# Optimization experiments

Measured on AMD Instinct MI355X. Metric: run time of the kernel, lower is better.

## Reference

```python
import jax, jax.numpy as jnp
from jax import lax
import numpy as np

B, N, C = 64, 8732, 81  # batch, anchors (SSD300), classes (COCO+bg)
POS_RATE = 0.003        # keep 3*num_pos < N (argsort column index must be in range)


def setup_inputs() -> dict:
    key = jax.random.key(0)
    k1, k2, k3, k4, k5, k6 = jax.random.split(key, 6)
    pred_conf = jax.random.normal(k1, (B, N, C), dtype=jnp.float32)
    pred_loc = jax.random.normal(k2, (B, N, 4), dtype=jnp.float32)
    # one-hot gt_conf; class 0 = background; sparse positives
    is_pos = jax.random.uniform(k3, (B, N)) < POS_RATE
    labels = jnp.where(is_pos, jax.random.randint(k4, (B, N), 1, C), 0)
    gt_conf = jax.nn.one_hot(labels, C, dtype=jnp.float32)
    gt_loc = jax.random.normal(k5, (B, N, 4), dtype=jnp.float32)
    return {"pred_conf": pred_conf, "pred_loc": pred_loc,
            "gt_conf": gt_conf, "gt_loc": gt_loc}


def reference(pred_conf, pred_loc, gt_conf, gt_loc):
    negative_ratio = 3.0
    # softmax cross entropy per anchor: [B, N]
    log_sm = jax.nn.log_softmax(pred_conf, axis=-1)
    conf_loss = -jnp.sum(log_sm * gt_conf, axis=-1)

    # positive mask (gt background prob == 0 => positive); detached in original
    pos_mask = (lax.stop_gradient(gt_conf)[:, :, 0] == 0).astype(jnp.float32)
    num_pos = jnp.sum(pos_mask)
    positive_conf_loss = pos_mask * conf_loss

    # hard-negative mining (faithful to original, including the quirk that the
    # "threshold" is the argsort INDEX value at column num_negative_conf)
    neg_mask = 1.0 - pos_mask
    cl_neg = lax.stop_gradient(conf_loss) * neg_mask  # detached in original
    order = jnp.argsort(cl_neg, axis=-1)              # [B, N] ascending
    num_neg = (negative_ratio * num_pos).astype(jnp.int32)  # scalar, traced
    idx = jnp.broadcast_to(num_neg, (cl_neg.shape[0], 1))
    thr = jnp.take_along_axis(order, idx, axis=1).astype(jnp.float32)  # [B,1]
    neg_mask = neg_mask * (cl_neg > thr).astype(jnp.float32)
    negative_conf_loss = neg_mask * conf_loss

    conf_total = jnp.sum(positive_conf_loss + negative_conf_loss, axis=-1)  # [B]

    # smooth-L1-ish loc loss (faithful, incl. loc_loss_mask == linear mask bug)
    d = pred_loc - gt_loc
    lin = (jnp.abs(lax.stop_gradient(d)) > 1.0).astype(jnp.float32)
    loc = ((jnp.abs(d) - 0.5) * lin + 0.5 * d * d * (1.0 - lin)) * lin
    loc_total = jnp.sum(loc, axis=(-1, -2))  # [B]

    return conf_total, loc_total
```

## Files before the change

kernel.cpp:

```cpp
#include <hip/hip_runtime.h>
#include <hip/hip_bf16.h>
#include <math.h>

#define NCLS 81
#define NANCH 8732
#define NB 64
#define TILE_A 64
#define TILE_FLOATS (TILE_A * NCLS)
#define NBUCKET 64
#define BUCKET_STRIDE 16

__global__ __launch_bounds__(256) void conf_kernel(
    const float* __restrict__ pred_conf,
    const float* __restrict__ gt_conf,
    float* __restrict__ val_out,
    int* __restrict__ pos_buckets)
{
    __shared__ float sp[TILE_FLOATS];
    __shared__ float sg[TILE_FLOATS];
    __shared__ int pcnt[4];
    const int tid = threadIdx.x;
    const long long tile = blockIdx.x;
    const long long base = tile * (long long)TILE_FLOATS;

    const float4* p4 = (const float4*)(pred_conf + base);
    const float4* g4 = (const float4*)(gt_conf + base);
    float4* sp4 = (float4*)sp;
    float4* sg4 = (float4*)sg;
#pragma unroll
    for (int i = 0; i < 6; ++i) {
        int idx = tid + i * 256;
        if (idx < TILE_FLOATS / 4) {
            sp4[idx] = p4[idx];
            sg4[idx] = g4[idx];
        }
    }
    __syncthreads();

    const int a = tid >> 2;
    const int q = tid & 3;
    const float* xrow = sp + a * NCLS;
    const float* grow = sg + a * NCLS;

    float x[21];
    float m = -INFINITY;
#pragma unroll
    for (int j = 0; j < 21; ++j) {
        int c = q + 4 * j;
        x[j] = (c < NCLS) ? xrow[c] : -INFINITY;
        m = fmaxf(m, x[j]);
    }
    m = fmaxf(m, __shfl_xor(m, 1));
    m = fmaxf(m, __shfl_xor(m, 2));

    float s = 0.f;
#pragma unroll
    for (int j = 0; j < 21; ++j) {
        int c = q + 4 * j;
        if (c < NCLS) s += expf(x[j] - m);
    }
    s += __shfl_xor(s, 1);
    s += __shfl_xor(s, 2);
    const float lse = m + logf(s);

    float dot = 0.f;
#pragma unroll
    for (int j = 0; j < 21; ++j) {
        int c = q + 4 * j;
        if (c < NCLS) dot += (x[j] - lse) * grow[c];
    }
    dot += __shfl_xor(dot, 1);
    dot += __shfl_xor(dot, 2);
    const float conf_loss = -dot;

    bool pos = false;
    if (q == 0) {
        pos = (grow[0] == 0.0f);
        val_out[tile * TILE_A + a] = pos ? -conf_loss : conf_loss;
    }
    unsigned long long mb = __ballot(pos);
    if ((tid & 63) == 0) pcnt[tid >> 6] = (int)__popcll(mb);
    __syncthreads();
    if (tid == 0) {
        int tot = pcnt[0] + pcnt[1] + pcnt[2] + pcnt[3];
        if (tot)
            atomicAdd(&pos_buckets[(blockIdx.x & (NBUCKET - 1)) * BUCKET_STRIDE], tot);
    }
}

__global__ __launch_bounds__(256) void loc_kernel(
    const float* __restrict__ pred_loc,
    const float* __restrict__ gt_loc,
    float* __restrict__ out)
{
    __shared__ float red[4];
    const int b = blockIdx.y;
    const int idx = blockIdx.x * 256 + threadIdx.x;
    float local = 0.f;
    if (idx < NANCH) {
        const float4* p = (const float4*)(pred_loc + (long long)b * (NANCH * 4));
        const float4* g = (const float4*)(gt_loc + (long long)b * (NANCH * 4));
        float4 pv = p[idx];
        float4 gv = g[idx];
        float d0 = pv.x - gv.x, d1 = pv.y - gv.y, d2 = pv.z - gv.z, d3 = pv.w - gv.w;
        float a0 = fabsf(d0), a1 = fabsf(d1), a2 = fabsf(d2), a3 = fabsf(d3);
        local  = (a0 > 1.f) ? (a0 - 0.5f) : 0.f;
        local += (a1 > 1.f) ? (a1 - 0.5f) : 0.f;
        local += (a2 > 1.f) ? (a2 - 0.5f) : 0.f;
        local += (a3 > 1.f) ? (a3 - 0.5f) : 0.f;
    }
    for (int off = 32; off; off >>= 1) local += __shfl_xor(local, off);
    if ((threadIdx.x & 63) == 0) red[threadIdx.x >> 6] = local;
    __syncthreads();
    if (threadIdx.x == 0)
        atomicAdd(&out[64 + b], red[0] + red[1] + red[2] + red[3]);
}

__global__ __launch_bounds__(256) void select_kernel(
    const float* __restrict__ val,
    const int* __restrict__ pos_buckets,
    float* __restrict__ out)
{
    __shared__ float cl[NANCH];
    __shared__ int hist[256];
    __shared__ int wsum[4];
    __shared__ int sh_numpos;
    __shared__ unsigned int sh_prefix;
    __shared__ int sh_k, sh_thr;
    __shared__ float red[4];

    const int b = blockIdx.x;
    const int tid = threadIdx.x;
    const int lane = tid & 63, w = tid >> 6;
    const float* row = val + (long long)b * NANCH;

    if (tid < 64) {
        int v = pos_buckets[tid * BUCKET_STRIDE];
        for (int off = 32; off; off >>= 1) v += __shfl_xor(v, off);
        if (tid == 0) sh_numpos = v;
    }

    float pos_local = 0.f;
    for (int i = tid; i < NANCH; i += 256) {
        float v = row[i];
        cl[i] = fmaxf(v, 0.0f);
        if (v < 0.f) pos_local -= v;
    }
    __syncthreads();

    int k = 3 * sh_numpos;
    if (k > NANCH - 1) k = NANCH - 1;
    if (k < 0) k = 0;

    unsigned int prefix = 0u;
    for (int r = 0; r < 4; ++r) {
        const int shift = 24 - 8 * r;
        const unsigned int maskHigh = (r == 0) ? 0u : (0xFFFFFFFFu << (shift + 8));
        hist[tid] = 0;
        __syncthreads();
        for (int i = tid; i < NANCH; i += 256) {
            unsigned int u = __float_as_uint(cl[i]);
            if ((u & maskHigh) == prefix)
                atomicAdd(&hist[(u >> shift) & 0xFF], 1);
        }
        __syncthreads();
        int h = hist[tid];
        int v = h;
#pragma unroll
        for (int off = 1; off < 64; off <<= 1) {
            int u2 = __shfl_up(v, off);
            if (lane >= off) v += u2;
        }
        if (lane == 63) wsum[w] = v;
        __syncthreads();
        int add = 0;
        for (int i = 0; i < w; ++i) add += wsum[i];
        int incl = v + add, excl = incl - h;
        if (excl <= k && k < incl) {
            sh_prefix = prefix | ((unsigned int)tid << shift);
            sh_k = k - excl;
        }
        __syncthreads();
        prefix = sh_prefix;
        k = sh_k;
        __syncthreads();
    }
    const unsigned int T = prefix;

    const int CHUNK = (NANCH + 255) / 256;
    const int lo = tid * CHUNK;
    const int hi = (lo + CHUNK < NANCH) ? (lo + CHUNK) : NANCH;
    int cnt = 0;
    for (int i = lo; i < hi; ++i)
        if (__float_as_uint(cl[i]) == T) ++cnt;
    {
        int v = cnt;
#pragma unroll
        for (int off = 1; off < 64; off <<= 1) {
            int u2 = __shfl_up(v, off);
            if (lane >= off) v += u2;
        }
        if (lane == 63) wsum[w] = v;
        __syncthreads();
        int add = 0;
        for (int i = 0; i < w; ++i) add += wsum[i];
        int incl = v + add, excl = incl - cnt;
        if (excl <= k && k < incl) {
            int need = k - excl, idx = NANCH - 1;
            for (int i = lo; i < hi; ++i) {
                if (__float_as_uint(cl[i]) == T) {
                    if (need == 0) { idx = i; break; }
                    --need;
                }
            }
            sh_thr = idx;
        }
        __syncthreads();
    }

    const float thr = (float)sh_thr;
    float local = pos_local;
    for (int i = tid; i < NANCH; i += 256) {
        float c = cl[i];
        if (c > thr) local += c;
    }
    for (int off = 32; off; off >>= 1) local += __shfl_xor(local, off);
    if ((tid & 63) == 0) red[tid >> 6] = local;
    __syncthreads();
    if (tid == 0) out[b] = red[0] + red[1] + red[2] + red[3];
}

extern "C" void kernel_launch(void* const* d_in, const int* in_sizes, int n_in,
                              void* d_out, int out_size, void* d_ws, size_t ws_size,
                              hipStream_t stream) {
    const float* pred_conf = (const float*)d_in[0];
    const float* pred_loc  = (const float*)d_in[1];
    const float* gt_conf   = (const float*)d_in[2];
    const float* gt_loc    = (const float*)d_in[3];
    float* out = (float*)d_out;

    int*   pos_buckets = (int*)d_ws;
    float* vals        = (float*)((char*)d_ws + 8192);

    hipMemsetAsync(d_ws, 0, 8192, stream);
    hipMemsetAsync(d_out, 0, 128 * sizeof(float), stream);

    conf_kernel<<<NB * NANCH / TILE_A, 256, 0, stream>>>(pred_conf, gt_conf, vals, pos_buckets);
    loc_kernel<<<dim3((NANCH + 255) / 256, NB), 256, 0, stream>>>(pred_loc, gt_loc, out);
    select_kernel<<<NB, 256, 0, stream>>>(vals, pos_buckets, out);
}
```

Measured before the change: 427.6 us.

## Drop LDS staging in conf kernel, atomically accumulate positive loss, widen select blocks

The conf kernel no longer stages tiles of pred_conf and gt_conf in shared memory. Each thread now reads its strided classes straight from global memory, which removes the LDS footprint and a barrier but gives up coalesced float4 loads. Positive-anchor losses are reduced per wavefront and added atomically into a per-row buffer, so the select kernel can load clean values without separating signs. The select kernel runs with 1024 threads per block to parallelise the radix-select passes across the 64 rows, at the cost of more barrier overhead.

New measurement: 404.3 us. 5.5% less time.

```diff
diff --git a/kernel.cpp b/kernel.cpp
--- a/kernel.cpp
+++ b/kernel.cpp
@@ -5,42 +5,20 @@
 #define NCLS 81
 #define NANCH 8732
 #define NB 64
-#define TILE_A 64
-#define TILE_FLOATS (TILE_A * NCLS)
-#define NBUCKET 64
 #define BUCKET_STRIDE 16
 
 __global__ __launch_bounds__(256) void conf_kernel(
     const float* __restrict__ pred_conf,
     const float* __restrict__ gt_conf,
-    float* __restrict__ val_out,
-    int* __restrict__ pos_buckets)
+    float* __restrict__ cl_out,
+    int* __restrict__ pos_buckets,
+    float* __restrict__ row_pos)
 {
-    __shared__ float sp[TILE_FLOATS];
-    __shared__ float sg[TILE_FLOATS];
-    __shared__ int pcnt[4];
     const int tid = threadIdx.x;
-    const long long tile = blockIdx.x;
-    const long long base = tile * (long long)TILE_FLOATS;
-
-    const float4* p4 = (const float4*)(pred_conf + base);
-    const float4* g4 = (const float4*)(gt_conf + base);
-    float4* sp4 = (float4*)sp;
-    float4* sg4 = (float4*)sg;
-#pragma unroll
-    for (int i = 0; i < 6; ++i) {
-        int idx = tid + i * 256;
-        if (idx < TILE_FLOATS / 4) {
-            sp4[idx] = p4[idx];
-            sg4[idx] = g4[idx];
-        }
-    }
-    __syncthreads();
-
-    const int a = tid >> 2;
+    const int anchor = blockIdx.x * 64 + (tid >> 2);
     const int q = tid & 3;
-    const float* xrow = sp + a * NCLS;
-    const float* grow = sg + a * NCLS;
+    const float* xrow = pred_conf + (size_t)anchor * NCLS;
+    const float* grow = gt_conf + (size_t)anchor * NCLS;
 
     float x[21];
     float m = -INFINITY;
@@ -63,28 +41,37 @@
     s += __shfl_xor(s, 2);
     const float lse = m + logf(s);
 
-    float dot = 0.f;
+    float dot = 0.f, g0 = 1.f;
 #pragma unroll
     for (int j = 0; j < 21; ++j) {
         int c = q + 4 * j;
-        if (c < NCLS) dot += (x[j] - lse) * grow[c];
+        if (c < NCLS) {
+            float g = grow[c];
+            if (c == 0) g0 = g;
+            dot = fmaf(g, x[j] - lse, dot);
+        }
     }
     dot += __shfl_xor(dot, 1);
     dot += __shfl_xor(dot, 2);
     const float conf_loss = -dot;
 
-    bool pos = false;
-    if (q == 0) {
-        pos = (grow[0] == 0.0f);
-        val_out[tile * TILE_A + a] = pos ? -conf_loss : conf_loss;
-    }
-    unsigned long long mb = __ballot(pos);
-    if ((tid & 63) == 0) pcnt[tid >> 6] = (int)__popcll(mb);
-    __syncthreads();
-    if (tid == 0) {
-        int tot = pcnt[0] + pcnt[1] + pcnt[2] + pcnt[3];
-        if (tot)
-            atomicAdd(&pos_buckets[(blockIdx.x & (NBUCKET - 1)) * BUCKET_STRIDE], tot);
+    const bool posf = (q == 0) && (g0 == 0.0f);
+    if (q == 0) cl_out[anchor] = posf ? 0.0f : conf_loss;
+
+    const int b = anchor / NANCH;
+    const float contrib = posf ? conf_loss : 0.0f;
+    const int bF = __builtin_amdgcn_readfirstlane(b);
+    float c0 = (b == bF) ? contrib : 0.0f;
+    float c1 = contrib - c0;
+    for (int off = 32; off; off >>= 1) {
+        c0 += __shfl_xor(c0, off);
+        c1 += __shfl_xor(c1, off);
+    }
+    const int pc = (int)__popcll(__ballot(posf));
+    if ((tid & 63) == 0) {
+        if (c0 != 0.f) atomicAdd(&row_pos[bF], c0);
+        if (c1 != 0.f) atomicAdd(&row_pos[bF + 1], c1);
+        if (pc) atomicAdd(&pos_buckets[(blockIdx.x & 63) * BUCKET_STRIDE], pc);
     }
 }
 
@@ -102,8 +89,8 @@
         const float4* g = (const float4*)(gt_loc + (long long)b * (NANCH * 4));
         float4 pv = p[idx];
         float4 gv = g[idx];
-        float d0 = pv.x - gv.x, d1 = pv.y - gv.y, d2 = pv.z - gv.z, d3 = pv.w - gv.w;
-        float a0 = fabsf(d0), a1 = fabsf(d1), a2 = fabsf(d2), a3 = fabsf(d3);
+        float a0 = fabsf(pv.x - gv.x), a1 = fabsf(pv.y - gv.y);
+        float a2 = fabsf(pv.z - gv.z), a3 = fabsf(pv.w - gv.w);
         local  = (a0 > 1.f) ? (a0 - 0.5f) : 0.f;
         local += (a1 > 1.f) ? (a1 - 0.5f) : 0.f;
         local += (a2 > 1.f) ? (a2 - 0.5f) : 0.f;
@@ -116,36 +103,31 @@
         atomicAdd(&out[64 + b], red[0] + red[1] + red[2] + red[3]);
 }
 
-__global__ __launch_bounds__(256) void select_kernel(
+__global__ __launch_bounds__(1024) void select_kernel(
     const float* __restrict__ val,
     const int* __restrict__ pos_buckets,
+    const float* __restrict__ row_pos,
     float* __restrict__ out)
 {
     __shared__ float cl[NANCH];
     __shared__ int hist[256];
-    __shared__ int wsum[4];
+    __shared__ int wsum[16];
+    __shared__ float fred[16];
     __shared__ int sh_numpos;
     __shared__ unsigned int sh_prefix;
     __shared__ int sh_k, sh_thr;
-    __shared__ float red[4];
 
     const int b = blockIdx.x;
     const int tid = threadIdx.x;
     const int lane = tid & 63, w = tid >> 6;
-    const float* row = val + (long long)b * NANCH;
+    const float* row = val + b * NANCH;
 
     if (tid < 64) {
         int v = pos_buckets[tid * BUCKET_STRIDE];
         for (int off = 32; off; off >>= 1) v += __shfl_xor(v, off);
         if (tid == 0) sh_numpos = v;
     }
-
-    float pos_local = 0.f;
-    for (int i = tid; i < NANCH; i += 256) {
-        float v = row[i];
-        cl[i] = fmaxf(v, 0.0f);
-        if (v < 0.f) pos_local -= v;
-    }
+    for (int i = tid; i < NANCH; i += 1024) cl[i] = row[i];
     __syncthreads();
 
     int k = 3 * sh_numpos;
@@ -156,29 +138,34 @@
     for (int r = 0; r < 4; ++r) {
         const int shift = 24 - 8 * r;
         const unsigned int maskHigh = (r == 0) ? 0u : (0xFFFFFFFFu << (shift + 8));
-        hist[tid] = 0;
-        __syncthreads();
-        for (int i = tid; i < NANCH; i += 256) {
+        if (tid < 256) hist[tid] = 0;
+        __syncthreads();
+        for (int i = tid; i < NANCH; i += 1024) {
             unsigned int u = __float_as_uint(cl[i]);
             if ((u & maskHigh) == prefix)
                 atomicAdd(&hist[(u >> shift) & 0xFF], 1);
         }
         __syncthreads();
-        int h = hist[tid];
-        int v = h;
-#pragma unroll
-        for (int off = 1; off < 64; off <<= 1) {
-            int u2 = __shfl_up(v, off);
-            if (lane >= off) v += u2;
-        }
-        if (lane == 63) wsum[w] = v;
-        __syncthreads();
-        int add = 0;
-        for (int i = 0; i < w; ++i) add += wsum[i];
-        int incl = v + add, excl = incl - h;
-        if (excl <= k && k < incl) {
-            sh_prefix = prefix | ((unsigned int)tid << shift);
-            sh_k = k - excl;
+        int h = 0, v = 0;
+        if (tid < 256) {
+            h = hist[tid];
+            v = h;
+#pragma unroll
+            for (int off = 1; off < 64; off <<= 1) {
+                int u2 = __shfl_up(v, off);
+                if (lane >= off) v += u2;
+            }
+            if (lane == 63) wsum[w] = v;
+        }
+        __syncthreads();
+        if (tid < 256) {
+            int add = 0;
+            for (int i = 0; i < w; ++i) add += wsum[i];
+            int incl = v + add, excl = incl - h;
+            if (excl <= k && k < incl) {
+                sh_prefix = prefix | ((unsigned int)tid << shift);
+                sh_k = k - excl;
+            }
         }
         __syncthreads();
         prefix = sh_prefix;
@@ -187,24 +174,33 @@
     }
     const unsigned int T = prefix;
 
-    const int CHUNK = (NANCH + 255) / 256;
-    const int lo = tid * CHUNK;
-    const int hi = (lo + CHUNK < NANCH) ? (lo + CHUNK) : NANCH;
+    const int CHUNK = 9;
+    int lo = tid * CHUNK; if (lo > NANCH) lo = NANCH;
+    int hi = lo + CHUNK; if (hi > NANCH) hi = NANCH;
     int cnt = 0;
     for (int i = lo; i < hi; ++i)
-        if (__float_as_uint(cl[i]) == T) ++cnt;
+        cnt += (__float_as_uint(cl[i]) == T);
+    int v2 = cnt;
+#pragma unroll
+    for (int off = 1; off < 64; off <<= 1) {
+        int u2 = __shfl_up(v2, off);
+        if (lane >= off) v2 += u2;
+    }
+    if (lane == 63) wsum[w] = v2;
+    __syncthreads();
+    if (tid < 16) {
+        int s = wsum[tid];
+#pragma unroll
+        for (int off = 1; off < 16; off <<= 1) {
+            int u2 = __shfl_up(s, off);
+            if (lane >= off) s += u2;
+        }
+        wsum[tid] = s;
+    }
+    __syncthreads();
     {
-        int v = cnt;
-#pragma unroll
-        for (int off = 1; off < 64; off <<= 1) {
-            int u2 = __shfl_up(v, off);
-            if (lane >= off) v += u2;
-        }
-        if (lane == 63) wsum[w] = v;
-        __syncthreads();
-        int add = 0;
-        for (int i = 0; i < w; ++i) add += wsum[i];
-        int incl = v + add, excl = incl - cnt;
+        int add = (w == 0) ? 0 : wsum[w - 1];
+        int incl = v2 + add, excl = incl - cnt;
         if (excl <= k && k < incl) {
             int need = k - excl, idx = NANCH - 1;
             for (int i = lo; i < hi; ++i) {
@@ -215,19 +211,23 @@
             }
             sh_thr = idx;
         }
-        __syncthreads();
-    }
+    }
+    __syncthreads();
 
     const float thr = (float)sh_thr;
-    float local = pos_local;
-    for (int i = tid; i < NANCH; i += 256) {
+    float local = 0.f;
+    for (int i = tid; i < NANCH; i += 1024) {
         float c = cl[i];
         if (c > thr) local += c;
     }
     for (int off = 32; off; off >>= 1) local += __shfl_xor(local, off);
-    if ((tid & 63) == 0) red[tid >> 6] = local;
-    __syncthreads();
-    if (tid == 0) out[b] = red[0] + red[1] + red[2] + red[3];
+    if (lane == 0) fred[w] = local;
+    __syncthreads();
+    if (tid == 0) {
+        float t = row_pos[b];
+        for (int i = 0; i < 16; ++i) t += fred[i];
+        out[b] = t;
+    }
 }
 
 extern "C" void kernel_launch(void* const* d_in, const int* in_sizes, int n_in,
@@ -240,12 +240,14 @@
     float* out = (float*)d_out;
 
     int*   pos_buckets = (int*)d_ws;
+    float* row_pos     = (float*)((char*)d_ws + 4096);
     float* vals        = (float*)((char*)d_ws + 8192);
 
     hipMemsetAsync(d_ws, 0, 8192, stream);
     hipMemsetAsync(d_out, 0, 128 * sizeof(float), stream);
 
-    conf_kernel<<<NB * NANCH / TILE_A, 256, 0, stream>>>(pred_conf, gt_conf, vals, pos_buckets);
+    conf_kernel<<<NB * NANCH / 64, 256, 0, stream>>>(pred_conf, gt_conf, vals,
+                                                     pos_buckets, row_pos);
     loc_kernel<<<dim3((NANCH + 255) / 256, NB), 256, 0, stream>>>(pred_loc, gt_loc, out);
-    select_kernel<<<NB, 256, 0, stream>>>(vals, pos_buckets, out);
-}
+    select_kernel<<<NB, 1024, 0, stream>>>(vals, pos_buckets, row_pos, out);
+}
```
